# Kernel tuning notes

Hardware: AMD Instinct MI355X
Metric: run time of the kernel (lower is better)

The kernel has to match this reference:

```python
import jax, jax.numpy as jnp
import numpy as np

BS, QLEN, DIM, NH = 4, 2048, 1024, 16
DH = DIM // NH
NEG = float(np.finfo(np.float32).min)


def setup_inputs() -> dict:
    key = jax.random.key(0)
    ks = jax.random.split(key, 10)
    s = 1.0 / np.sqrt(DIM)
    return {
        "hidden_states": jax.random.normal(ks[0], (BS, QLEN, DIM), jnp.float32),
        "attention_mask": jnp.ones((BS, QLEN), jnp.int32),
        "Wq": jax.random.normal(ks[1], (DIM, DIM), jnp.float32) * s,
        "bq": jnp.zeros((DIM,), jnp.float32),
        "Wk": jax.random.normal(ks[2], (DIM, DIM), jnp.float32) * s,
        "bk": jnp.zeros((DIM,), jnp.float32),
        "Wv": jax.random.normal(ks[3], (DIM, DIM), jnp.float32) * s,
        "bv": jnp.zeros((DIM,), jnp.float32),
        "Wo": jax.random.normal(ks[4], (DIM, DIM), jnp.float32) * s,
        "bo": jnp.zeros((DIM,), jnp.float32),
    }


def _heads(x, bs):
    # [bs, len, dim] -> [bs, n_heads, len, dim_per_head]
    return x.reshape(bs, -1, NH, DH).transpose(0, 2, 1, 3)


def reference(hidden_states, attention_mask, Wq, bq, Wk, bk, Wv, bv, Wo, bo):
    bs, qlen, dim = hidden_states.shape
    q = _heads(hidden_states @ Wq.T + bq, bs) / jnp.sqrt(jnp.asarray(DH, hidden_states.dtype))
    k = _heads(hidden_states @ Wk.T + bk, bs)
    v = _heads(hidden_states @ Wv.T + bv, bs)
    scores = jnp.einsum("bhqd,bhkd->bhqk", q, k)  # [bs, nh, qlen, klen]
    mask = (attention_mask == 0)[:, None, None, :]  # [bs,1,1,klen]
    scores = jnp.where(mask, NEG, scores)
    weights = jax.nn.softmax(scores.astype(jnp.float32), axis=-1).astype(scores.dtype)
    context = jnp.einsum("bhqk,bhkd->bhqd", weights, v)
    context = context.transpose(0, 2, 1, 3).reshape(bs, qlen, dim)
    return context @ Wo.T + bo
```

## Files before the change

### kernel.cpp

```cpp
#include <hip/hip_runtime.h>
#include <hip/hip_bf16.h>

#define BS 4
#define QLEN 2048
#define DIM 1024
#define NH 16
#define DH 64

typedef __attribute__((ext_vector_type(8))) short bf16x8;
typedef __attribute__((ext_vector_type(4))) float f32x4;
typedef __attribute__((ext_vector_type(16))) float f32x16;
typedef __attribute__((ext_vector_type(2))) unsigned int u32x2;
typedef __attribute__((ext_vector_type(4))) unsigned int u32x4;
typedef unsigned short u16;
typedef unsigned int u32;
typedef unsigned long long u64;

#define LOG2E 1.44269504088896f

__device__ __forceinline__ u32 cvtpk_bf16(float lo, float hi) {
    u32 r;
    asm("v_cvt_pk_bf16_f32 %0, %1, %2" : "=v"(r) : "v"(lo), "v"(hi));
    return r;
}
__device__ __forceinline__ u16 f2bf_hw(float f) { return (u16)cvtpk_bf16(f, f); }

__device__ __forceinline__ void async_lds16(const void* gp, void* lp) {
    __builtin_amdgcn_global_load_lds(
        (const __attribute__((address_space(1))) u32*)(u64)gp,
        (__attribute__((address_space(3))) u32*)(u32)(u64)lp,
        16, 0, 0);
}

__global__ void cvt_fused(const float* __restrict__ H,
                          const float* __restrict__ W0, const float* __restrict__ W1,
                          const float* __restrict__ W2, const float* __restrict__ W3,
                          u16* __restrict__ Hb,
                          u16* __restrict__ D0, u16* __restrict__ D1,
                          u16* __restrict__ D2, u16* __restrict__ D3) {
    const int h4 = (BS * QLEN * DIM) / 4;
    int i = blockIdx.x * blockDim.x + threadIdx.x;
    const float* s;
    u16* d;
    int off;
    if (i < h4) { s = H; d = Hb; off = i; }
    else {
        int j = i - h4;
        int ws = j >> 18;
        off = j & 262143;
        s = ws == 0 ? W0 : ws == 1 ? W1 : ws == 2 ? W2 : W3;
        d = ws == 0 ? D0 : ws == 1 ? D1 : ws == 2 ? D2 : D3;
    }
    float4 v = ((const float4*)s)[off];
    uint2 o;
    o.x = cvtpk_bf16(v.x, v.y);
    o.y = cvtpk_bf16(v.z, v.w);
    ((uint2*)d)[off] = o;
}

__global__ void mask_prep(const int* __restrict__ mask, float* __restrict__ maskF,
                          int* __restrict__ flags) {
    const int tile = blockIdx.x;
    const int lane = threadIdx.x;
    const int idx = tile * 64 + lane;
    const int v = mask[idx];
    maskF[idx] = v ? 1.0f : 0.0f;
    u64 bal = __ballot(v == 0);
    if (lane == 0) flags[tile] = (bal != 0ull) ? 1 : 0;
}

__global__ __launch_bounds__(256) void gemm_qkv(
    const u16* __restrict__ Hb,
    const u16* __restrict__ Wq, const u16* __restrict__ Wk, const u16* __restrict__ Wv,
    const float* __restrict__ bq, const float* __restrict__ bk, const float* __restrict__ bvv,
    u16* __restrict__ Qb, u16* __restrict__ Kb, u16* __restrict__ Vt)
{
    __shared__ __align__(16) u16 As[128 * 32];
    __shared__ __align__(16) u16 Bs[128 * 32];
    const int z = blockIdx.z;
    const u16* W = z == 0 ? Wq : z == 1 ? Wk : Wv;
    const float* bias = z == 0 ? bq : z == 1 ? bk : bvv;
    const int t = threadIdx.x;
    const int w = t >> 6, lane = t & 63;
    const int lr = lane & 15, lg = lane >> 4;
    const int m0 = blockIdx.y * 128, n0 = blockIdx.x * 128;
    const int wm = (w >> 1) * 64, wn = (w & 1) * 64;
    const int srow = w * 16 + (lane >> 2);
    const int sk = (lane & 3) * 8;

    f32x4 acc[4][4] = {};

    for (int kt = 0; kt < DIM; kt += 32) {
        __syncthreads();
        async_lds16(Hb + (u64)(m0 + srow) * DIM + kt + sk,      &As[(w * 16) * 32]);
        async_lds16(Hb + (u64)(m0 + 64 + srow) * DIM + kt + sk, &As[(64 + w * 16) * 32]);
        async_lds16(W + (u64)(n0 + srow) * DIM + kt + sk,       &Bs[(w * 16) * 32]);
        async_lds16(W + (u64)(n0 + 64 + srow) * DIM + kt + sk,  &Bs[(64 + w * 16) * 32]);
        __syncthreads();
        bf16x8 a[4], b[4];
#pragma unroll
        for (int i = 0; i < 4; ++i) a[i] = *(const bf16x8*)&As[(wm + i * 16 + lr) * 32 + lg * 8];
#pragma unroll
        for (int i = 0; i < 4; ++i) b[i] = *(const bf16x8*)&Bs[(wn + i * 16 + lr) * 32 + lg * 8];
#pragma unroll
        for (int mi = 0; mi < 4; ++mi)
#pragma unroll
            for (int ni = 0; ni < 4; ++ni)
                acc[mi][ni] = __builtin_amdgcn_mfma_f32_16x16x32_bf16(a[mi], b[ni], acc[mi][ni], 0, 0, 0);
    }

#pragma unroll
    for (int mi = 0; mi < 4; ++mi)
#pragma unroll
        for (int ni = 0; ni < 4; ++ni) {
            const int col = n0 + wn + ni * 16 + lr;
            const float bb = bias[col];
#pragma unroll
            for (int r = 0; r < 4; ++r) {
                const int row = m0 + wm + mi * 16 + lg * 4 + r;
                const float v = acc[mi][ni][r] + bb;
                const int bh = (row >> 11) * NH + (col >> 6);
                const int q = row & (QLEN - 1);
                const int d = col & (DH - 1);
                if (z == 0)      Qb[((u64)bh * QLEN + q) * DH + d] = f2bf_hw(v * (0.125f * LOG2E));
                else if (z == 1) Kb[((u64)bh * QLEN + q) * DH + d] = f2bf_hw(v);
                else             Vt[((u64)bh * DH + d) * QLEN + q] = f2bf_hw(v);
            }
        }
}

__global__ __launch_bounds__(256) void gemm_o(
    const u16* __restrict__ A, const u16* __restrict__ W,
    const float* __restrict__ bias, float* __restrict__ ofp)
{
    __shared__ __align__(16) u16 As[128 * 32];
    __shared__ __align__(16) u16 Bs[128 * 32];
    const int t = threadIdx.x;
    const int w = t >> 6, lane = t & 63;
    const int lr = lane & 15, lg = lane >> 4;
    const int m0 = blockIdx.y * 128, n0 = blockIdx.x * 128;
    const int wm = (w >> 1) * 64, wn = (w & 1) * 64;
    const int srow = w * 16 + (lane >> 2);
    const int sk = (lane & 3) * 8;

    f32x4 acc[4][4] = {};

    for (int kt = 0; kt < DIM; kt += 32) {
        __syncthreads();
        async_lds16(A + (u64)(m0 + srow) * DIM + kt + sk,      &As[(w * 16) * 32]);
        async_lds16(A + (u64)(m0 + 64 + srow) * DIM + kt + sk, &As[(64 + w * 16) * 32]);
        async_lds16(W + (u64)(n0 + srow) * DIM + kt + sk,      &Bs[(w * 16) * 32]);
        async_lds16(W + (u64)(n0 + 64 + srow) * DIM + kt + sk, &Bs[(64 + w * 16) * 32]);
        __syncthreads();
        bf16x8 a[4], b[4];
#pragma unroll
        for (int i = 0; i < 4; ++i) a[i] = *(const bf16x8*)&As[(wm + i * 16 + lr) * 32 + lg * 8];
#pragma unroll
        for (int i = 0; i < 4; ++i) b[i] = *(const bf16x8*)&Bs[(wn + i * 16 + lr) * 32 + lg * 8];
#pragma unroll
        for (int mi = 0; mi < 4; ++mi)
#pragma unroll
            for (int ni = 0; ni < 4; ++ni)
                acc[mi][ni] = __builtin_amdgcn_mfma_f32_16x16x32_bf16(a[mi], b[ni], acc[mi][ni], 0, 0, 0);
    }

#pragma unroll
    for (int mi = 0; mi < 4; ++mi)
#pragma unroll
        for (int ni = 0; ni < 4; ++ni) {
            const int col = n0 + wn + ni * 16 + lr;
            const float bb = bias[col];
#pragma unroll
            for (int r = 0; r < 4; ++r) {
                const int row = m0 + wm + mi * 16 + lg * 4 + r;
                ofp[(u64)row * DIM + col] = acc[mi][ni][r] + bb;
            }
        }
}

__global__ __launch_bounds__(512) void attn_kernel(
    const u16* __restrict__ Qb, const u16* __restrict__ Kb, const u16* __restrict__ Vt,
    const float* __restrict__ maskF, const int* __restrict__ mflags, u16* __restrict__ ctx)
{
    __shared__ __align__(16) u16 Ks[4][64 * 64];
    __shared__ __align__(16) u16 Vs[4][64 * 64];

    const int t = threadIdx.x;
    const int w = t >> 6, lane = t & 63;
    const int l5 = lane & 31, hi = lane >> 5, l7 = lane & 7;

    const int id = blockIdx.x + 8 * blockIdx.y;
    const int v = (id & 7) * 64 + (id >> 3);
    const int qt = v & 7, bh = v >> 3;
    const int b = bh >> 4, hh = bh & 15;
    const int q0 = qt * 256;

    const u16* Kbh = Kb + (u64)bh * QLEN * DH;
    const u16* Vth = Vt + (u64)bh * DH * QLEN;
    const float* mFb = maskF + b * QLEN;
    const int* flb = mflags + b * (QLEN / 64);

    const u64 fmask = __ballot(flb[lane & 31] != 0);

    const u16* qp = Qb + ((u64)bh * QLEN + q0 + w * 32 + l5) * DH + hi * 8;
    bf16x8 bq[4];
#pragma unroll
    for (int dc = 0; dc < 4; ++dc) bq[dc] = *(const bf16x8*)(qp + dc * 16);

    f32x16 o[2] = {};
    float mrun = -3.0e38f, lsum = 0.f;

    const int srow = w * 8 + (lane >> 3);
    const int sch = l7 ^ (srow & 7);

    auto STAGE = [&](int B, int KT) {
        async_lds16(Kbh + (u64)(KT * 64 + srow) * DH + sch * 8, &Ks[B][(w * 8) * 64]);
        async_lds16(Vth + (u64)srow * QLEN + KT * 64 + sch * 8, &Vs[B][(w * 8) * 64]);
    };

    auto compute = [&](int B, int kt64) {
        const char* Kbase = (const char*)&Ks[B][0];
        const char* Vbase = (const char*)&Vs[B][0];

        f32x16 s[2] = {};
        __builtin_amdgcn_s_setprio(1);
#pragma unroll
        for (int dc = 0; dc < 4; ++dc) {
            const u32 off = (u32)(l5 * 128) + (u32)(((2 * dc + hi) ^ l7) << 4);
            bf16x8 ak0 = *(const bf16x8*)(Kbase + off);
            bf16x8 ak1 = *(const bf16x8*)(Kbase + off + 4096);
            s[0] = __builtin_amdgcn_mfma_f32_32x32x16_bf16(ak0, bq[dc], s[0], 0, 0, 0);
            s[1] = __builtin_amdgcn_mfma_f32_32x32x16_bf16(ak1, bq[dc], s[1], 0, 0, 0);
        }
        __builtin_amdgcn_s_setprio(0);

        bf16x8 av0[4], av1[4];
#pragma unroll
        for (int kc = 0; kc < 4; ++kc) {
            const u32 voff = (u32)(l5 * 128) + (u32)(((2 * kc + hi) ^ l7) << 4);
            av0[kc] = *(const bf16x8*)(Vbase + voff);
            av1[kc] = *(const bf16x8*)(Vbase + voff + 4096);
        }

        float mx[16];
#pragma unroll
        for (int i = 0; i < 16; ++i) mx[i] = fmaxf(s[0][i], s[1][i]);
#pragma unroll
        for (int st = 8; st > 0; st >>= 1)
#pragma unroll
            for (int i = 0; i < 16; ++i) if (i < st) mx[i] = fmaxf(mx[i], mx[i + st]);
        const float tma = fmaxf(mx[0], __shfl_xor(mx[0], 32));

        if (!__all(tma <= mrun + 11.5415603f)) {
            const float nm = fmaxf(mrun, tma);
            const float corr = exp2f(mrun - nm);
            mrun = nm;
            lsum *= corr;
#pragma unroll
            for (int i = 0; i < 16; ++i) { o[0][i] *= corr; o[1][i] *= corr; }
        }

#pragma unroll
        for (int i = 0; i < 16; ++i) {
            s[0][i] = exp2f(s[0][i] - mrun);
            s[1][i] = exp2f(s[1][i] - mrun);
        }

        if ((fmask >> kt64) & 1ull) {
#pragma unroll
            for (int kb = 0; kb < 2; ++kb)
#pragma unroll
                for (int m = 0; m < 4; ++m) {
                    float4 mm = *(const float4*)&mFb[kt64 * 64 + kb * 32 + m * 8 + hi * 4];
                    s[kb][4 * m + 0] *= mm.x;
                    s[kb][4 * m + 1] *= mm.y;
                    s[kb][4 * m + 2] *= mm.z;
                    s[kb][4 * m + 3] *= mm.w;
                }
        }

        {
            float ps[16];
#pragma unroll
            for (int i = 0; i < 16; ++i) ps[i] = s[0][i] + s[1][i];
#pragma unroll
            for (int st = 8; st > 0; st >>= 1)
#pragma unroll
                for (int i = 0; i < 16; ++i) if (i < st) ps[i] += ps[i + st];
            lsum += ps[0];
        }

        __builtin_amdgcn_s_setprio(1);
#pragma unroll
        for (int kc = 0; kc < 4; ++kc) {
            const int kb = kc >> 1;
            const int base = 8 * (kc & 1);
            const u32 P00 = cvtpk_bf16(s[kb][base + 0], s[kb][base + 1]);
            const u32 P01 = cvtpk_bf16(s[kb][base + 2], s[kb][base + 3]);
            const u32 P10 = cvtpk_bf16(s[kb][base + 4], s[kb][base + 5]);
            const u32 P11 = cvtpk_bf16(s[kb][base + 6], s[kb][base + 7]);
            u32x2 w02 = __builtin_amdgcn_permlane32_swap(P00, P10, false, false);
            u32x2 w13 = __builtin_amdgcn_permlane32_swap(P01, P11, false, false);
            u32x4 words;
            words.x = w02[0]; words.y = w13[0]; words.z = w02[1]; words.w = w13[1];
            const bf16x8 bp = __builtin_bit_cast(bf16x8, words);

            o[0] = __builtin_amdgcn_mfma_f32_32x32x16_bf16(av0[kc], bp, o[0], 0, 0, 0);
            o[1] = __builtin_amdgcn_mfma_f32_32x32x16_bf16(av1[kc], bp, o[1], 0, 0, 0);
        }
        __builtin_amdgcn_s_setprio(0);
    };

    STAGE(0, 0);
    STAGE(1, 1);
    for (int tt = 0; tt < 30; ++tt) {
        STAGE((tt + 2) & 3, tt + 2);
        asm volatile("s_waitcnt vmcnt(4)" ::: "memory");
        __builtin_amdgcn_s_barrier();
        __builtin_amdgcn_sched_barrier(0);
        compute(tt & 3, tt);
    }
    asm volatile("s_waitcnt vmcnt(2)" ::: "memory");
    __builtin_amdgcn_s_barrier();
    __builtin_amdgcn_sched_barrier(0);
    compute(30 & 3, 30);
    asm volatile("s_waitcnt vmcnt(0)" ::: "memory");
    __builtin_amdgcn_s_barrier();
    __builtin_amdgcn_sched_barrier(0);
    compute(31 & 3, 31);

    const float lall = lsum + __shfl_xor(lsum, 32);
    const float inv = 1.0f / fmaxf(lall, 1e-37f);

    u16* cp = ctx + (((u64)b * QLEN + (q0 + w * 32 + l5)) * NH + hh) * DH;
#pragma unroll
    for (int db = 0; db < 2; ++db)
#pragma unroll
        for (int m = 0; m < 4; ++m) {
            const int d0 = db * 32 + m * 8 + hi * 4;
            const u32 wA = cvtpk_bf16(o[db][4 * m + 0] * inv, o[db][4 * m + 1] * inv);
            const u32 wB = cvtpk_bf16(o[db][4 * m + 2] * inv, o[db][4 * m + 3] * inv);
            *(u32*)(cp + d0) = wA;
            *(u32*)(cp + d0 + 2) = wB;
        }
}

extern "C" void kernel_launch(void* const* d_in, const int* in_sizes, int n_in,
                              void* d_out, int out_size, void* d_ws, size_t ws_size,
                              hipStream_t stream) {
    const float* H    = (const float*)d_in[0];
    const int*   mask = (const int*)d_in[1];
    const float* Wq   = (const float*)d_in[2];
    const float* bq   = (const float*)d_in[3];
    const float* Wk   = (const float*)d_in[4];
    const float* bk   = (const float*)d_in[5];
    const float* Wv   = (const float*)d_in[6];
    const float* bv   = (const float*)d_in[7];
    const float* Wo   = (const float*)d_in[8];
    const float* bo   = (const float*)d_in[9];
    float* out = (float*)d_out;

    const u64 NTOK = (u64)BS * QLEN;
    const u64 HN = NTOK * DIM;
    const u64 WN = (u64)DIM * DIM;

    u16* Hb  = (u16*)d_ws;
    u16* Wqb = Hb + HN;
    u16* Wkb = Wqb + WN;
    u16* Wvb = Wkb + WN;
    u16* Wob = Wvb + WN;
    u16* Qb  = Wob + WN;
    u16* Kb  = Qb + HN;
    u16* Vtg = Kb + HN;
    u16* Ctx = Vtg + HN;
    float* maskF = (float*)(Ctx + HN);
    int* mflags = (int*)(maskF + BS * QLEN);

    cvt_fused<<<12288, 256, 0, stream>>>(H, Wq, Wk, Wv, Wo, Hb, Wqb, Wkb, Wvb, Wob);
    mask_prep<<<BS * (QLEN / 64), 64, 0, stream>>>(mask, maskF, mflags);

    gemm_qkv<<<dim3(DIM / 128, (int)(NTOK / 128), 3), 256, 0, stream>>>(
        Hb, Wqb, Wkb, Wvb, bq, bk, bv, Qb, Kb, Vtg);

    attn_kernel<<<dim3(QLEN / 256, BS * NH), 512, 0, stream>>>(Qb, Kb, Vtg, maskF, mflags, Ctx);

    gemm_o<<<dim3(DIM / 128, (int)(NTOK / 128)), 256, 0, stream>>>(Ctx, Wob, bo, out);
}
```

Before: 251.1 us.

## Process two 32-row query tiles per wave in attention to reuse K/V fragments

The attention block shrinks from 8 waves to 4, and each wave now handles 64 query rows as two 32-row sub-tiles with separate softmax state. The K and V fragments read from LDS are loaded once per tile and reused for both sub-tiles, which halves LDS read traffic per query row. Each thread now issues twice as many async staging loads, and the waitcnt thresholds are raised to match. The cost is roughly doubled accumulator and register use per wave and fewer waves per block, which may cut occupancy and latency hiding.

```diff
diff --git a/kernel.cpp b/kernel.cpp
--- a/kernel.cpp
+++ b/kernel.cpp
@@ -178,7 +178,7 @@
         }
 }
 
-__global__ __launch_bounds__(512) void attn_kernel(
+__global__ __launch_bounds__(256, 2) void attn_kernel(
     const u16* __restrict__ Qb, const u16* __restrict__ Kb, const u16* __restrict__ Vt,
     const float* __restrict__ maskF, const int* __restrict__ mflags, u16* __restrict__ ctx)
 {
@@ -202,125 +202,135 @@
 
     const u64 fmask = __ballot(flb[lane & 31] != 0);
 
-    const u16* qp = Qb + ((u64)bh * QLEN + q0 + w * 32 + l5) * DH + hi * 8;
-    bf16x8 bq[4];
-#pragma unroll
-    for (int dc = 0; dc < 4; ++dc) bq[dc] = *(const bf16x8*)(qp + dc * 16);
-
-    f32x16 o[2] = {};
-    float mrun = -3.0e38f, lsum = 0.f;
-
-    const int srow = w * 8 + (lane >> 3);
-    const int sch = l7 ^ (srow & 7);
+    bf16x8 bq[2][4];
+#pragma unroll
+    for (int qa = 0; qa < 2; ++qa) {
+        const u16* qp = Qb + ((u64)bh * QLEN + q0 + w * 64 + qa * 32 + l5) * DH + hi * 8;
+#pragma unroll
+        for (int dc = 0; dc < 4; ++dc) bq[qa][dc] = *(const bf16x8*)(qp + dc * 16);
+    }
+
+    f32x16 o[2][2] = {};
+    float mrun[2] = {-3.0e38f, -3.0e38f};
+    float lsum[2] = {0.f, 0.f};
 
     auto STAGE = [&](int B, int KT) {
-        async_lds16(Kbh + (u64)(KT * 64 + srow) * DH + sch * 8, &Ks[B][(w * 8) * 64]);
-        async_lds16(Vth + (u64)srow * QLEN + KT * 64 + sch * 8, &Vs[B][(w * 8) * 64]);
+#pragma unroll
+        for (int c = 0; c < 2; ++c) {
+            const int row = w * 16 + c * 8 + (lane >> 3);
+            const int ch = l7 ^ (row & 7);
+            async_lds16(Kbh + (u64)(KT * 64 + row) * DH + ch * 8, &Ks[B][(w * 16 + c * 8) * 64]);
+            async_lds16(Vth + (u64)row * QLEN + KT * 64 + ch * 8, &Vs[B][(w * 16 + c * 8) * 64]);
+        }
     };
 
     auto compute = [&](int B, int kt64) {
         const char* Kbase = (const char*)&Ks[B][0];
         const char* Vbase = (const char*)&Vs[B][0];
 
-        f32x16 s[2] = {};
-        __builtin_amdgcn_s_setprio(1);
+        bf16x8 ak0[4], ak1[4], av0[4], av1[4];
 #pragma unroll
         for (int dc = 0; dc < 4; ++dc) {
             const u32 off = (u32)(l5 * 128) + (u32)(((2 * dc + hi) ^ l7) << 4);
-            bf16x8 ak0 = *(const bf16x8*)(Kbase + off);
-            bf16x8 ak1 = *(const bf16x8*)(Kbase + off + 4096);
-            s[0] = __builtin_amdgcn_mfma_f32_32x32x16_bf16(ak0, bq[dc], s[0], 0, 0, 0);
-            s[1] = __builtin_amdgcn_mfma_f32_32x32x16_bf16(ak1, bq[dc], s[1], 0, 0, 0);
+            ak0[dc] = *(const bf16x8*)(Kbase + off);
+            ak1[dc] = *(const bf16x8*)(Kbase + off + 4096);
+            av0[dc] = *(const bf16x8*)(Vbase + off);
+            av1[dc] = *(const bf16x8*)(Vbase + off + 4096);
         }
+
+        f32x16 s[2][2] = {};
+        __builtin_amdgcn_s_setprio(1);
+#pragma unroll
+        for (int dc = 0; dc < 4; ++dc)
+#pragma unroll
+            for (int qa = 0; qa < 2; ++qa) {
+                s[qa][0] = __builtin_amdgcn_mfma_f32_32x32x16_bf16(ak0[dc], bq[qa][dc], s[qa][0], 0, 0, 0);
+                s[qa][1] = __builtin_amdgcn_mfma_f32_32x32x16_bf16(ak1[dc], bq[qa][dc], s[qa][1], 0, 0, 0);
+            }
         __builtin_amdgcn_s_setprio(0);
 
-        bf16x8 av0[4], av1[4];
-#pragma unroll
-        for (int kc = 0; kc < 4; ++kc) {
-            const u32 voff = (u32)(l5 * 128) + (u32)(((2 * kc + hi) ^ l7) << 4);
-            av0[kc] = *(const bf16x8*)(Vbase + voff);
-            av1[kc] = *(const bf16x8*)(Vbase + voff + 4096);
+#pragma unroll
+        for (int qa = 0; qa < 2; ++qa) {
+            float mx[16];
+#pragma unroll
+            for (int i = 0; i < 16; ++i) mx[i] = fmaxf(s[qa][0][i], s[qa][1][i]);
+#pragma unroll
+            for (int st = 8; st > 0; st >>= 1)
+#pragma unroll
+                for (int i = 0; i < 16; ++i) if (i < st) mx[i] = fmaxf(mx[i], mx[i + st]);
+            const float tma = fmaxf(mx[0], __shfl_xor(mx[0], 32));
+
+            if (!__all(tma <= mrun[qa] + 11.5415603f)) {
+                const float nm = fmaxf(mrun[qa], tma);
+                const float corr = exp2f(mrun[qa] - nm);
+                mrun[qa] = nm;
+                lsum[qa] *= corr;
+#pragma unroll
+                for (int i = 0; i < 16; ++i) { o[qa][0][i] *= corr; o[qa][1][i] *= corr; }
+            }
+
+#pragma unroll
+            for (int i = 0; i < 16; ++i) {
+                s[qa][0][i] = exp2f(s[qa][0][i] - mrun[qa]);
+                s[qa][1][i] = exp2f(s[qa][1][i] - mrun[qa]);
+            }
+
+            if ((fmask >> kt64) & 1ull) {
+#pragma unroll
+                for (int kb = 0; kb < 2; ++kb)
+#pragma unroll
+                    for (int m = 0; m < 4; ++m) {
+                        float4 mm = *(const float4*)&mFb[kt64 * 64 + kb * 32 + m * 8 + hi * 4];
+                        s[qa][kb][4 * m + 0] *= mm.x;
+                        s[qa][kb][4 * m + 1] *= mm.y;
+                        s[qa][kb][4 * m + 2] *= mm.z;
+                        s[qa][kb][4 * m + 3] *= mm.w;
+                    }
+            }
+
+            {
+                float ps[16];
+#pragma unroll
+                for (int i = 0; i < 16; ++i) ps[i] = s[qa][0][i] + s[qa][1][i];
+#pragma unroll
+                for (int st = 8; st > 0; st >>= 1)
+#pragma unroll
+                    for (int i = 0; i < 16; ++i) if (i < st) ps[i] += ps[i + st];
+                lsum[qa] += ps[0];
+            }
+
+            __builtin_amdgcn_s_setprio(1);
+#pragma unroll
+            for (int kc = 0; kc < 4; ++kc) {
+                const int kb = kc >> 1;
+                const int base = 8 * (kc & 1);
+                const u32 P00 = cvtpk_bf16(s[qa][kb][base + 0], s[qa][kb][base + 1]);
+                const u32 P01 = cvtpk_bf16(s[qa][kb][base + 2], s[qa][kb][base + 3]);
+                const u32 P10 = cvtpk_bf16(s[qa][kb][base + 4], s[qa][kb][base + 5]);
+                const u32 P11 = cvtpk_bf16(s[qa][kb][base + 6], s[qa][kb][base + 7]);
+                u32x2 w02 = __builtin_amdgcn_permlane32_swap(P00, P10, false, false);
+                u32x2 w13 = __builtin_amdgcn_permlane32_swap(P01, P11, false, false);
+                u32x4 words;
+                words.x = w02[0]; words.y = w13[0]; words.z = w02[1]; words.w = w13[1];
+                const bf16x8 bp = __builtin_bit_cast(bf16x8, words);
+
+                o[qa][0] = __builtin_amdgcn_mfma_f32_32x32x16_bf16(av0[kc], bp, o[qa][0], 0, 0, 0);
+                o[qa][1] = __builtin_amdgcn_mfma_f32_32x32x16_bf16(av1[kc], bp, o[qa][1], 0, 0, 0);
+            }
+            __builtin_amdgcn_s_setprio(0);
         }
-
-        float mx[16];
-#pragma unroll
-        for (int i = 0; i < 16; ++i) mx[i] = fmaxf(s[0][i], s[1][i]);
-#pragma unroll
-        for (int st = 8; st > 0; st >>= 1)
-#pragma unroll
-            for (int i = 0; i < 16; ++i) if (i < st) mx[i] = fmaxf(mx[i], mx[i + st]);
-        const float tma = fmaxf(mx[0], __shfl_xor(mx[0], 32));
-
-        if (!__all(tma <= mrun + 11.5415603f)) {
-            const float nm = fmaxf(mrun, tma);
-            const float corr = exp2f(mrun - nm);
-            mrun = nm;
-            lsum *= corr;
-#pragma unroll
-            for (int i = 0; i < 16; ++i) { o[0][i] *= corr; o[1][i] *= corr; }
-        }
-
-#pragma unroll
-        for (int i = 0; i < 16; ++i) {
-            s[0][i] = exp2f(s[0][i] - mrun);
-            s[1][i] = exp2f(s[1][i] - mrun);
-        }
-
-        if ((fmask >> kt64) & 1ull) {
-#pragma unroll
-            for (int kb = 0; kb < 2; ++kb)
-#pragma unroll
-                for (int m = 0; m < 4; ++m) {
-                    float4 mm = *(const float4*)&mFb[kt64 * 64 + kb * 32 + m * 8 + hi * 4];
-                    s[kb][4 * m + 0] *= mm.x;
-                    s[kb][4 * m + 1] *= mm.y;
-                    s[kb][4 * m + 2] *= mm.z;
-                    s[kb][4 * m + 3] *= mm.w;
-                }
-        }
-
-        {
-            float ps[16];
-#pragma unroll
-            for (int i = 0; i < 16; ++i) ps[i] = s[0][i] + s[1][i];
-#pragma unroll
-            for (int st = 8; st > 0; st >>= 1)
-#pragma unroll
-                for (int i = 0; i < 16; ++i) if (i < st) ps[i] += ps[i + st];
-            lsum += ps[0];
-        }
-
-        __builtin_amdgcn_s_setprio(1);
-#pragma unroll
-        for (int kc = 0; kc < 4; ++kc) {
-            const int kb = kc >> 1;
-            const int base = 8 * (kc & 1);
-            const u32 P00 = cvtpk_bf16(s[kb][base + 0], s[kb][base + 1]);
-            const u32 P01 = cvtpk_bf16(s[kb][base + 2], s[kb][base + 3]);
-            const u32 P10 = cvtpk_bf16(s[kb][base + 4], s[kb][base + 5]);
-            const u32 P11 = cvtpk_bf16(s[kb][base + 6], s[kb][base + 7]);
-            u32x2 w02 = __builtin_amdgcn_permlane32_swap(P00, P10, false, false);
-            u32x2 w13 = __builtin_amdgcn_permlane32_swap(P01, P11, false, false);
-            u32x4 words;
-            words.x = w02[0]; words.y = w13[0]; words.z = w02[1]; words.w = w13[1];
-            const bf16x8 bp = __builtin_bit_cast(bf16x8, words);
-
-            o[0] = __builtin_amdgcn_mfma_f32_32x32x16_bf16(av0[kc], bp, o[0], 0, 0, 0);
-            o[1] = __builtin_amdgcn_mfma_f32_32x32x16_bf16(av1[kc], bp, o[1], 0, 0, 0);
-        }
-        __builtin_amdgcn_s_setprio(0);
     };
 
     STAGE(0, 0);
     STAGE(1, 1);
     for (int tt = 0; tt < 30; ++tt) {
         STAGE((tt + 2) & 3, tt + 2);
-        asm volatile("s_waitcnt vmcnt(4)" ::: "memory");
+        asm volatile("s_waitcnt vmcnt(8)" ::: "memory");
         __builtin_amdgcn_s_barrier();
         __builtin_amdgcn_sched_barrier(0);
         compute(tt & 3, tt);
     }
-    asm volatile("s_waitcnt vmcnt(2)" ::: "memory");
+    asm volatile("s_waitcnt vmcnt(4)" ::: "memory");
     __builtin_amdgcn_s_barrier();
     __builtin_amdgcn_sched_barrier(0);
     compute(30 & 3, 30);
@@ -329,20 +339,23 @@
     __builtin_amdgcn_sched_barrier(0);
     compute(31 & 3, 31);
 
-    const float lall = lsum + __shfl_xor(lsum, 32);
-    const float inv = 1.0f / fmaxf(lall, 1e-37f);
-
-    u16* cp = ctx + (((u64)b * QLEN + (q0 + w * 32 + l5)) * NH + hh) * DH;
-#pragma unroll
-    for (int db = 0; db < 2; ++db)
-#pragma unroll
-        for (int m = 0; m < 4; ++m) {
-            const int d0 = db * 32 + m * 8 + hi * 4;
-            const u32 wA = cvtpk_bf16(o[db][4 * m + 0] * inv, o[db][4 * m + 1] * inv);
-            const u32 wB = cvtpk_bf16(o[db][4 * m + 2] * inv, o[db][4 * m + 3] * inv);
-            *(u32*)(cp + d0) = wA;
-            *(u32*)(cp + d0 + 2) = wB;
-        }
+#pragma unroll
+    for (int qa = 0; qa < 2; ++qa) {
+        const float lall = lsum[qa] + __shfl_xor(lsum[qa], 32);
+        const float inv = 1.0f / fmaxf(lall, 1e-37f);
+
+        u16* cp = ctx + (((u64)b * QLEN + (q0 + w * 64 + qa * 32 + l5)) * NH + hh) * DH;
+#pragma unroll
+        for (int db = 0; db < 2; ++db)
+#pragma unroll
+            for (int m = 0; m < 4; ++m) {
+                const int d0 = db * 32 + m * 8 + hi * 4;
+                const u32 wA = cvtpk_bf16(o[qa][db][4 * m + 0] * inv, o[qa][db][4 * m + 1] * inv);
+                const u32 wB = cvtpk_bf16(o[qa][db][4 * m + 2] * inv, o[qa][db][4 * m + 3] * inv);
+                *(u32*)(cp + d0) = wA;
+                *(u32*)(cp + d0 + 2) = wB;
+            }
+    }
 }
 
 extern "C" void kernel_launch(void* const* d_in, const int* in_sizes, int n_in,
@@ -382,7 +395,7 @@
     gemm_qkv<<<dim3(DIM / 128, (int)(NTOK / 128), 3), 256, 0, stream>>>(
         Hb, Wqb, Wkb, Wvb, bq, bk, bv, Qb, Kb, Vtg);
 
-    attn_kernel<<<dim3(QLEN / 256, BS * NH), 512, 0, stream>>>(Qb, Kb, Vtg, maskF, mflags, Ctx);
+    attn_kernel<<<dim3(QLEN / 256, BS * NH), 256, 0, stream>>>(Qb, Kb, Vtg, maskF, mflags, Ctx);
 
     gemm_o<<<dim3(DIM / 128, (int)(NTOK / 128)), 256, 0, stream>>>(Ctx, Wob, bo, out);
 }
```

Result: no change. 253.2 us (+0.9%).
